# Kernel tuning notes

Measured on AMD Instinct MI355X. Metric: run time of the kernel, lower is better.

## Reference

```python
import jax, jax.numpy as jnp
import numpy as np


def setup_inputs() -> dict:
    key = jax.random.key(0)
    k1, k2 = jax.random.split(key)
    B, N, M, D = 4, 8192, 8192, 3
    preds = jax.random.normal(k1, (B, M, D), dtype=jnp.float32)
    gts = jax.random.normal(k2, (B, N, D), dtype=jnp.float32)
    return {"preds": preds, "gts": gts, "c": 1}


def reference(preds, gts, c):
    # x = gts [B, Nx, D], y = preds [B, Ny, D] (matches batch_pairwise_dist(gts, preds))
    x, y = gts, preds
    cf = jnp.asarray(c, dtype=x.dtype)
    # P[b, i, j] = ||x_i||^2 + ||y_j||^2 - 2 <x_i, y_j>  (squared Euclidean distance)
    zz = jnp.einsum('bnd,bmd->bnm', x, y)            # [B, Nx, Ny]
    rx = jnp.sum(x * x, axis=-1)[:, :, None]          # [B, Nx, 1]
    ry = jnp.sum(y * y, axis=-1)[:, None, :]          # [B, 1, Ny]
    P = rx + ry - 2.0 * zz                            # [B, Nx, Ny]

    def huber(v):
        return jnp.where(v < cf, 0.5 * v * v, cf * v - 0.5 * cf * cf)

    loss_1 = jnp.sum(huber(jnp.min(P, axis=1)))       # min over Nx (gts side)
    loss_2 = jnp.sum(huber(jnp.min(P, axis=2)))       # min over Ny (preds side)
    return loss_1 + loss_2
```

## Files before the change

kernel.cpp:

```cpp
#include <hip/hip_runtime.h>
#include <math.h>

typedef _Float16 f16x8 __attribute__((ext_vector_type(8)));
typedef float f32x16 __attribute__((ext_vector_type(16)));

#define TILE 1024

__device__ __forceinline__ float decode_scalar(const int* p) {
    int i = *p;
    if (i > -16777216 && i < 16777216) return (float)i;
    return __int_as_float(i);
}
__device__ __forceinline__ float min3f(float a, float b, float c) {
    float d;
    asm("v_min3_f32 %0, %1, %2, %3" : "=v"(d) : "v"(a), "v"(b), "v"(c));
    return d;
}

__device__ __forceinline__ f16x8 make_afrag(float x, float y, float z, int half) {
    const float rn = fmaf(x, x, fmaf(y, y, z * z));
    const float ax = -2.f * x, ay = -2.f * y, az = -2.f * z;
    const _Float16 ahx = (_Float16)ax, ahy = (_Float16)ay, ahz = (_Float16)az;
    const _Float16 alx = (_Float16)(ax - (float)ahx);
    const _Float16 aly = (_Float16)(ay - (float)ahy);
    const _Float16 alz = (_Float16)(az - (float)ahz);
    const _Float16 rh = (_Float16)rn, rl = (_Float16)(rn - (float)rh);
    const _Float16 one = (_Float16)1.f;
    if (half == 0) return (f16x8){ahx, ahy, ahz, alx, aly, alz, ahx, ahy};
    return (f16x8){ahz, alx, aly, alz, rh, rl, one, one};
}
__device__ __forceinline__ void make_bfrags(float x, float y, float z,
                                            f16x8* b0, f16x8* b1) {
    const float rn = fmaf(x, x, fmaf(y, y, z * z));
    const _Float16 bhx = (_Float16)x, bhy = (_Float16)y, bhz = (_Float16)z;
    const _Float16 blx = (_Float16)(x - (float)bhx);
    const _Float16 bly = (_Float16)(y - (float)bhy);
    const _Float16 blz = (_Float16)(z - (float)bhz);
    const _Float16 rh = (_Float16)rn, rl = (_Float16)(rn - (float)rh);
    const _Float16 one = (_Float16)1.f;
    *b0 = (f16x8){bhx, bhy, bhz, bhx, bhy, bhz, blx, bly};
    *b1 = (f16x8){blz, blx, bly, blz, one, one, rh, rl};
}

__global__ __launch_bounds__(256) void nn_mfma(
    const float* __restrict__ preds, const float* __restrict__ gts,
    int M, int N, int B, int rsplit, int Qstride, float* __restrict__ part)
{
    const int zc    = blockIdx.z;
    const int dir   = zc / rsplit;
    const int chunk = zc - dir * rsplit;
    const int b     = blockIdx.y;

    const int Q = dir ? N : M;
    const int R = dir ? M : N;
    const float* __restrict__ qraw = (dir ? gts : preds) + (size_t)b * Q * 3;
    const float* __restrict__ rraw = (dir ? preds : gts) + (size_t)b * R * 3;

    const int q0blk = blockIdx.x * 256;
    if (q0blk >= Q) return;
    const int tid  = threadIdx.x;
    const int lane = tid & 63, w = tid >> 6;
    const int q0   = q0blk + w * 64;
    const int lrow = lane & 31, lh = lane >> 5;

    float ax = 0.f, ay = 0.f, az = 0.f, bx = 0.f, by = 0.f, bz = 0.f;
    const int qa = q0 + lrow, qb = q0 + 32 + lrow;
    if (qa < Q) { const float* s = qraw + (size_t)qa * 3; ax = s[0]; ay = s[1]; az = s[2]; }
    if (qb < Q) { const float* s = qraw + (size_t)qb * 3; bx = s[0]; by = s[1]; bz = s[2]; }
    const f16x8 af0 = make_afrag(ax, ay, az, lh);
    const f16x8 af1 = make_afrag(bx, by, bz, lh);

    __shared__ f16x8 sB[TILE * 2];

    f32x16 rm0, rm1;
    #pragma unroll
    for (int j = 0; j < 16; ++j) { rm0[j] = INFINITY; rm1[j] = INFINITY; }

    const int tilesTotal = (R + TILE - 1) / TILE;
    const int tpc = (tilesTotal + rsplit - 1) / rsplit;
    const int t0 = chunk * tpc;
    const int t1 = min(tilesTotal, t0 + tpc);

    for (int tt = t0; tt < t1; ++tt) {
        const int s0 = tt * TILE;
        __syncthreads();
        #pragma unroll
        for (int k = 0; k < 4; ++k) {
            const int p  = tid + k * 256;
            const int gi = s0 + p;
            f16x8 b0, b1;
            if (gi < R) {
                const float* s = rraw + (size_t)gi * 3;
                make_bfrags(s[0], s[1], s[2], &b0, &b1);
            } else {
                const _Float16 z0 = (_Float16)0.f, one = (_Float16)1.f;
                const _Float16 big = (_Float16)60000.f;
                b0 = (f16x8){z0, z0, z0, z0, z0, z0, z0, z0};
                b1 = (f16x8){z0, z0, z0, z0, one, one, big, z0};
            }
            const int g = p >> 5, sl = p & 31;
            sB[g * 64 + sl]      = b0;
            sB[g * 64 + 32 + sl] = b1;
        }
        __syncthreads();

        #pragma unroll 1
        for (int tp = 0; tp < TILE / 64; ++tp) {
            const f16x8 cb0 = sB[2 * tp * 64 + lane];
            const f16x8 cb1 = sB[(2 * tp + 1) * 64 + lane];
            f32x16 dA, dB;
            asm volatile(
                "v_mfma_f32_32x32x16_f16 %0, %2, %3, 0\n\t"
                "v_mfma_f32_32x32x16_f16 %1, %2, %4, 0\n\t"
                "s_nop 7\n\t"
                "s_nop 7\n\t"
                "s_nop 7\n\t"
                "s_nop 7"
                : "=&v"(dA), "=&v"(dB)
                : "v"(af0), "v"(cb0), "v"(cb1));
            #pragma unroll
            for (int j = 0; j < 16; ++j) rm0[j] = min3f(dA[j], dB[j], rm0[j]);
            f32x16 dC, dD;
            asm volatile(
                "v_mfma_f32_32x32x16_f16 %0, %2, %3, 0\n\t"
                "v_mfma_f32_32x32x16_f16 %1, %2, %4, 0\n\t"
                "s_nop 7\n\t"
                "s_nop 7\n\t"
                "s_nop 7\n\t"
                "s_nop 7"
                : "=&v"(dC), "=&v"(dD)
                : "v"(af1), "v"(cb0), "v"(cb1));
            #pragma unroll
            for (int j = 0; j < 16; ++j) rm1[j] = min3f(dC[j], dD[j], rm1[j]);
        }
    }

    __syncthreads();
    float* sT = (float*)&sB[0] + (w << 11);
    const int c  = lrow;
    const int sw = 4 * (c & 7);

    #pragma unroll
    for (int jj = 0; jj < 4; ++jj) {
        const int qb0 = jj * 8 + 4 * lh;
        float4 v0 = { rm0[4*jj], rm0[4*jj+1], rm0[4*jj+2], rm0[4*jj+3] };
        *(float4*)&sT[c * 64 + (qb0 ^ sw)] = v0;
        const int qb1 = 32 + qb0;
        float4 v1 = { rm1[4*jj], rm1[4*jj+1], rm1[4*jj+2], rm1[4*jj+3] };
        *(float4*)&sT[c * 64 + (qb1 ^ sw)] = v1;
    }
    __syncthreads();

    float t16[16];
    #pragma unroll
    for (int cc = 0; cc < 16; ++cc) {
        const float va = sT[(2*cc)     * 64 + (lane ^ (4 * ((2*cc)     & 7)))];
        const float vb = sT[(2*cc + 1) * 64 + (lane ^ (4 * ((2*cc + 1) & 7)))];
        t16[cc] = fminf(va, vb);
    }
    #pragma unroll
    for (int s = 8; s > 0; s >>= 1)
        #pragma unroll
        for (int i = 0; i < 8; ++i)
            if (i < s) t16[i] = fminf(t16[i], t16[i + s]);

    const size_t pbase = (((size_t)dir * B + b) * rsplit + chunk) * (size_t)Qstride + q0;
    part[pbase + lane] = t16[0];
}

__global__ __launch_bounds__(1024) void huber_reduce(
    const float* __restrict__ part, const int* __restrict__ cptr,
    int M, int N, int B, int rsplit, int Qstride, float* __restrict__ out)
{
    const int dir = blockIdx.z;
    const int b   = blockIdx.y;
    const int Q   = dir ? N : M;
    const int tid = threadIdx.x;
    const int j   = blockIdx.x * 1024 + tid;

    float h = 0.f;
    if (j < Q) {
        const size_t base = (((size_t)dir * B + b) * rsplit) * (size_t)Qstride + j;
        float v = part[base];
        #pragma unroll 4
        for (int k = 1; k < rsplit; ++k) v = fminf(v, part[base + (size_t)k * Qstride]);
        const float c = decode_scalar(cptr);
        h = (v < c) ? (0.5f * v * v) : fmaf(c, v, -0.5f * c * c);
    }

    #pragma unroll
    for (int off = 32; off > 0; off >>= 1) h += __shfl_down(h, off, 64);

    __shared__ float wsum[16];
    if ((tid & 63) == 0) wsum[tid >> 6] = h;
    __syncthreads();
    if (tid < 64) {
        float t = (tid < 16) ? wsum[tid] : 0.f;
        #pragma unroll
        for (int off = 8; off > 0; off >>= 1) t += __shfl_down(t, off, 64);
        if (tid == 0) atomicAdd(out, t);
    }
}

extern "C" void kernel_launch(void* const* d_in, const int* in_sizes, int n_in,
                              void* d_out, int out_size, void* d_ws, size_t ws_size,
                              hipStream_t stream) {
    const float* preds = (const float*)d_in[0];
    const float* gts   = (const float*)d_in[1];
    const int*   cptr  = (const int*)d_in[2];

    const int B = 4, D = 3;
    const int M = in_sizes[0] / (B * D);
    const int N = in_sizes[1] / (B * D);
    const int Qmax = (M > N) ? M : N;
    const int Qstride = (Qmax + 255) & ~255;
    const int rsplit = 4;

    float* part = (float*)d_ws;
    hipMemsetAsync(d_out, 0, (size_t)out_size * sizeof(float), stream);

    dim3 g1(Qstride / 256, B, 2 * rsplit);
    nn_mfma<<<g1, 256, 0, stream>>>(preds, gts, M, N, B, rsplit, Qstride, part);

    dim3 g2((Qmax + 1023) / 1024, B, 2);
    huber_reduce<<<g2, 1024, 0, stream>>>(part, cptr, M, N, B, rsplit, Qstride,
                                          (float*)d_out);
}
```

Baseline: 33.21 us.

## Software-pipeline MFMA tile loop so min3 reductions overlap next MFMAs

Restructures the inner tile loop so the MFMA outputs of one step are min-reduced while the next step's MFMAs are in flight. It adds a prologue and epilogue and drops the hard-coded s_nop padding after each MFMA pair. Scheduling barriers fix the ordering of shared-memory loads, min3 reductions and MFMA issue. The aim is to remove idle cycles spent waiting on MFMA results. The risk is that hazard wait-states are no longer guaranteed for inline-asm MFMA results read soon after issue, especially in the epilogue, and the extra live accumulators raise register pressure.

```diff
diff --git a/kernel.cpp b/kernel.cpp
--- a/kernel.cpp
+++ b/kernel.cpp
@@ -16,6 +16,7 @@
     asm("v_min3_f32 %0, %1, %2, %3" : "=v"(d) : "v"(a), "v"(b), "v"(c));
     return d;
 }
+#define SBAR() __builtin_amdgcn_sched_barrier(0)
 
 __device__ __forceinline__ f16x8 make_afrag(float x, float y, float z, int half) {
     const float rn = fmaf(x, x, fmaf(y, y, z * z));
@@ -104,35 +105,45 @@
         }
         __syncthreads();
 
+        const f16x8* pl = sB + lane;
+        f16x8 cb0 = pl[0];
+        f16x8 cb1 = pl[64];
+        f32x16 dA, dB, dC, dD;
+        asm volatile(
+            "v_mfma_f32_32x32x16_f16 %0, %2, %3, 0\n\t"
+            "v_mfma_f32_32x32x16_f16 %1, %2, %4, 0"
+            : "=&v"(dA), "=&v"(dB) : "v"(af0), "v"(cb0), "v"(cb1));
+        asm volatile(
+            "v_mfma_f32_32x32x16_f16 %0, %2, %3, 0\n\t"
+            "v_mfma_f32_32x32x16_f16 %1, %2, %4, 0"
+            : "=&v"(dC), "=&v"(dD) : "v"(af1), "v"(cb0), "v"(cb1));
+
         #pragma unroll 1
-        for (int tp = 0; tp < TILE / 64; ++tp) {
-            const f16x8 cb0 = sB[2 * tp * 64 + lane];
-            const f16x8 cb1 = sB[(2 * tp + 1) * 64 + lane];
-            f32x16 dA, dB;
+        for (int tp = 1; tp < TILE / 64; ++tp) {
+            SBAR();
+            cb0 = pl[tp * 128];
+            cb1 = pl[tp * 128 + 64];
+            #pragma unroll
+            for (int j = 0; j < 16; ++j) rm0[j] = min3f(dA[j], dB[j], rm0[j]);
+            SBAR();
             asm volatile(
                 "v_mfma_f32_32x32x16_f16 %0, %2, %3, 0\n\t"
-                "v_mfma_f32_32x32x16_f16 %1, %2, %4, 0\n\t"
-                "s_nop 7\n\t"
-                "s_nop 7\n\t"
-                "s_nop 7\n\t"
-                "s_nop 7"
-                : "=&v"(dA), "=&v"(dB)
-                : "v"(af0), "v"(cb0), "v"(cb1));
+                "v_mfma_f32_32x32x16_f16 %1, %2, %4, 0"
+                : "=&v"(dA), "=&v"(dB) : "v"(af0), "v"(cb0), "v"(cb1));
+            SBAR();
             #pragma unroll
-            for (int j = 0; j < 16; ++j) rm0[j] = min3f(dA[j], dB[j], rm0[j]);
-            f32x16 dC, dD;
+            for (int j = 0; j < 16; ++j) rm1[j] = min3f(dC[j], dD[j], rm1[j]);
+            SBAR();
             asm volatile(
                 "v_mfma_f32_32x32x16_f16 %0, %2, %3, 0\n\t"
-                "v_mfma_f32_32x32x16_f16 %1, %2, %4, 0\n\t"
-                "s_nop 7\n\t"
-                "s_nop 7\n\t"
-                "s_nop 7\n\t"
-                "s_nop 7"
-                : "=&v"(dC), "=&v"(dD)
-                : "v"(af1), "v"(cb0), "v"(cb1));
-            #pragma unroll
-            for (int j = 0; j < 16; ++j) rm1[j] = min3f(dC[j], dD[j], rm1[j]);
+                "v_mfma_f32_32x32x16_f16 %1, %2, %4, 0"
+                : "=&v"(dC), "=&v"(dD) : "v"(af1), "v"(cb0), "v"(cb1));
         }
+        SBAR();
+        #pragma unroll
+        for (int j = 0; j < 16; ++j) rm0[j] = min3f(dA[j], dB[j], rm0[j]);
+        #pragma unroll
+        for (int j = 0; j < 16; ++j) rm1[j] = min3f(dC[j], dD[j], rm1[j]);
     }
 
     __syncthreads();
```

After: 31.56 us (median of 2 runs). -5.0%, faster.

## Load reference points directly per wave with register prefetch instead of LDS tiles

Applied to the files above, without the earlier changes.

The shared-memory tiling of reference-point fragments is replaced. Each wave now reads two reference points per iteration straight from global memory, prefetches the next pair into registers, and packs the f16 hi/lo fragments in-lane. This removes the block-wide barriers and LDS traffic around each tile, and a barrier in the final per-wave transpose is dropped. The cost is that all four waves now repeat the packing arithmetic and issue redundant strided global loads that depend on cache hits. The split of the reference set across chunks is now done at 64-point granularity.

```diff
diff --git a/kernel.cpp b/kernel.cpp
--- a/kernel.cpp
+++ b/kernel.cpp
@@ -3,8 +3,6 @@
 
 typedef _Float16 f16x8 __attribute__((ext_vector_type(8)));
 typedef float f32x16 __attribute__((ext_vector_type(16)));
-
-#define TILE 1024
 
 __device__ __forceinline__ float decode_scalar(const int* p) {
     int i = *p;
@@ -29,17 +27,19 @@
     if (half == 0) return (f16x8){ahx, ahy, ahz, alx, aly, alz, ahx, ahy};
     return (f16x8){ahz, alx, aly, alz, rh, rl, one, one};
 }
-__device__ __forceinline__ void make_bfrags(float x, float y, float z,
-                                            f16x8* b0, f16x8* b1) {
-    const float rn = fmaf(x, x, fmaf(y, y, z * z));
+
+__device__ __forceinline__ f16x8 pack_lane(float x, float y, float z,
+                                           int oob, int lh) {
+    float rn = fmaf(x, x, fmaf(y, y, z * z));
+    rn = oob ? 60000.f : rn;
     const _Float16 bhx = (_Float16)x, bhy = (_Float16)y, bhz = (_Float16)z;
     const _Float16 blx = (_Float16)(x - (float)bhx);
     const _Float16 bly = (_Float16)(y - (float)bhy);
     const _Float16 blz = (_Float16)(z - (float)bhz);
     const _Float16 rh = (_Float16)rn, rl = (_Float16)(rn - (float)rh);
     const _Float16 one = (_Float16)1.f;
-    *b0 = (f16x8){bhx, bhy, bhz, bhx, bhy, bhz, blx, bly};
-    *b1 = (f16x8){blz, blx, bly, blz, one, one, rh, rl};
+    if (lh == 0) return (f16x8){bhx, bhy, bhz, bhx, bhy, bhz, blx, bly};
+    return (f16x8){blz, blx, bly, blz, one, one, rh, rl};
 }
 
 __global__ __launch_bounds__(256) void nn_mfma(
@@ -56,11 +56,9 @@
     const float* __restrict__ qraw = (dir ? gts : preds) + (size_t)b * Q * 3;
     const float* __restrict__ rraw = (dir ? preds : gts) + (size_t)b * R * 3;
 
-    const int q0blk = blockIdx.x * 256;
-    if (q0blk >= Q) return;
     const int tid  = threadIdx.x;
     const int lane = tid & 63, w = tid >> 6;
-    const int q0   = q0blk + w * 64;
+    const int q0   = blockIdx.x * 256 + w * 64;
     const int lrow = lane & 31, lh = lane >> 5;
 
     float ax = 0.f, ay = 0.f, az = 0.f, bx = 0.f, by = 0.f, bz = 0.f;
@@ -70,44 +68,39 @@
     const f16x8 af0 = make_afrag(ax, ay, az, lh);
     const f16x8 af1 = make_afrag(bx, by, bz, lh);
 
-    __shared__ f16x8 sB[TILE * 2];
+    __shared__ float sTall[4 * 2048];
 
     f32x16 rm0, rm1;
     #pragma unroll
     for (int j = 0; j < 16; ++j) { rm0[j] = INFINITY; rm1[j] = INFINITY; }
 
-    const int tilesTotal = (R + TILE - 1) / TILE;
-    const int tpc = (tilesTotal + rsplit - 1) / rsplit;
-    const int t0 = chunk * tpc;
-    const int t1 = min(tilesTotal, t0 + tpc);
-
-    for (int tt = t0; tt < t1; ++tt) {
-        const int s0 = tt * TILE;
-        __syncthreads();
-        #pragma unroll
-        for (int k = 0; k < 4; ++k) {
-            const int p  = tid + k * 256;
-            const int gi = s0 + p;
-            f16x8 b0, b1;
-            if (gi < R) {
-                const float* s = rraw + (size_t)gi * 3;
-                make_bfrags(s[0], s[1], s[2], &b0, &b1);
-            } else {
-                const _Float16 z0 = (_Float16)0.f, one = (_Float16)1.f;
-                const _Float16 big = (_Float16)60000.f;
-                b0 = (f16x8){z0, z0, z0, z0, z0, z0, z0, z0};
-                b1 = (f16x8){z0, z0, z0, z0, one, one, big, z0};
+    const int gran = (((R + 63) >> 6) + rsplit - 1) / rsplit;
+    const int g0 = chunk * gran;
+    const int iters = min(gran, ((R + 63) >> 6) - g0);
+
+    if (iters > 0) {
+        int pt = g0 * 64 + lrow;
+        int o0 = (pt >= R), o1 = (pt + 32 >= R);
+        const float* s0 = rraw + (size_t)min(pt, R - 1) * 3;
+        const float* s1 = rraw + (size_t)min(pt + 32, R - 1) * 3;
+        float cx0 = s0[0], cy0 = s0[1], cz0 = s0[2];
+        float cx1 = s1[0], cy1 = s1[1], cz1 = s1[2];
+
+        #pragma unroll 1
+        for (int tp = 0; tp < iters; ++tp) {
+            const float x0 = cx0, y0 = cy0, z0 = cz0;
+            const float x1 = cx1, y1 = cy1, z1 = cz1;
+            const int f0 = o0, f1 = o1;
+            if (tp + 1 < iters) {
+                pt += 64;
+                o0 = (pt >= R); o1 = (pt + 32 >= R);
+                const float* n0 = rraw + (size_t)min(pt, R - 1) * 3;
+                const float* n1 = rraw + (size_t)min(pt + 32, R - 1) * 3;
+                cx0 = n0[0]; cy0 = n0[1]; cz0 = n0[2];
+                cx1 = n1[0]; cy1 = n1[1]; cz1 = n1[2];
             }
-            const int g = p >> 5, sl = p & 31;
-            sB[g * 64 + sl]      = b0;
-            sB[g * 64 + 32 + sl] = b1;
-        }
-        __syncthreads();
-
-        #pragma unroll 1
-        for (int tp = 0; tp < TILE / 64; ++tp) {
-            const f16x8 cb0 = sB[2 * tp * 64 + lane];
-            const f16x8 cb1 = sB[(2 * tp + 1) * 64 + lane];
+            const f16x8 cb0 = pack_lane(x0, y0, z0, f0, lh);
+            const f16x8 cb1 = pack_lane(x1, y1, z1, f1, lh);
             f32x16 dA, dB;
             asm volatile(
                 "v_mfma_f32_32x32x16_f16 %0, %2, %3, 0\n\t"
@@ -135,8 +128,7 @@
         }
     }
 
-    __syncthreads();
-    float* sT = (float*)&sB[0] + (w << 11);
+    float* sT = sTall + (w << 11);
     const int c  = lrow;
     const int sw = 4 * (c & 7);
 
@@ -149,7 +141,6 @@
         float4 v1 = { rm1[4*jj], rm1[4*jj+1], rm1[4*jj+2], rm1[4*jj+3] };
         *(float4*)&sT[c * 64 + (qb1 ^ sw)] = v1;
     }
-    __syncthreads();
 
     float t16[16];
     #pragma unroll
```

Result: slower. 43.75 us (+31.7%).

## Halve query rows per wave to double block count in MFMA NN kernel

Applied to the files above, without the earlier changes.

Each wave now processes 32 query points with a single A fragment instead of 64 with two, and the grid doubles along x to cover the same queries. This halves the per-wave accumulator registers and MFMA work per reference tile, giving twice as many blocks to spread across CUs. In exchange, each staged reference tile in shared memory is reused by half as many queries, so tile building and LDS reads per MFMA roughly double.

```diff
diff --git a/kernel.cpp b/kernel.cpp
--- a/kernel.cpp
+++ b/kernel.cpp
@@ -56,25 +56,23 @@
     const float* __restrict__ qraw = (dir ? gts : preds) + (size_t)b * Q * 3;
     const float* __restrict__ rraw = (dir ? preds : gts) + (size_t)b * R * 3;
 
-    const int q0blk = blockIdx.x * 256;
+    const int q0blk = blockIdx.x * 128;
     if (q0blk >= Q) return;
     const int tid  = threadIdx.x;
     const int lane = tid & 63, w = tid >> 6;
-    const int q0   = q0blk + w * 64;
+    const int q0   = q0blk + w * 32;
     const int lrow = lane & 31, lh = lane >> 5;
 
-    float ax = 0.f, ay = 0.f, az = 0.f, bx = 0.f, by = 0.f, bz = 0.f;
-    const int qa = q0 + lrow, qb = q0 + 32 + lrow;
+    float ax = 0.f, ay = 0.f, az = 0.f;
+    const int qa = q0 + lrow;
     if (qa < Q) { const float* s = qraw + (size_t)qa * 3; ax = s[0]; ay = s[1]; az = s[2]; }
-    if (qb < Q) { const float* s = qraw + (size_t)qb * 3; bx = s[0]; by = s[1]; bz = s[2]; }
-    const f16x8 af0 = make_afrag(ax, ay, az, lh);
-    const f16x8 af1 = make_afrag(bx, by, bz, lh);
+    const f16x8 af = make_afrag(ax, ay, az, lh);
 
     __shared__ f16x8 sB[TILE * 2];
 
-    f32x16 rm0, rm1;
-    #pragma unroll
-    for (int j = 0; j < 16; ++j) { rm0[j] = INFINITY; rm1[j] = INFINITY; }
+    f32x16 rm;
+    #pragma unroll
+    for (int j = 0; j < 16; ++j) rm[j] = INFINITY;
 
     const int tilesTotal = (R + TILE - 1) / TILE;
     const int tpc = (tilesTotal + rsplit - 1) / rsplit;
@@ -104,10 +102,11 @@
         }
         __syncthreads();
 
+        const f16x8* pl = sB + lane;
         #pragma unroll 1
         for (int tp = 0; tp < TILE / 64; ++tp) {
-            const f16x8 cb0 = sB[2 * tp * 64 + lane];
-            const f16x8 cb1 = sB[(2 * tp + 1) * 64 + lane];
+            const f16x8 cb0 = pl[tp * 128];
+            const f16x8 cb1 = pl[tp * 128 + 64];
             f32x16 dA, dB;
             asm volatile(
                 "v_mfma_f32_32x32x16_f16 %0, %2, %3, 0\n\t"
@@ -117,45 +116,30 @@
                 "s_nop 7\n\t"
                 "s_nop 7"
                 : "=&v"(dA), "=&v"(dB)
-                : "v"(af0), "v"(cb0), "v"(cb1));
+                : "v"(af), "v"(cb0), "v"(cb1));
             #pragma unroll
-            for (int j = 0; j < 16; ++j) rm0[j] = min3f(dA[j], dB[j], rm0[j]);
-            f32x16 dC, dD;
-            asm volatile(
-                "v_mfma_f32_32x32x16_f16 %0, %2, %3, 0\n\t"
-                "v_mfma_f32_32x32x16_f16 %1, %2, %4, 0\n\t"
-                "s_nop 7\n\t"
-                "s_nop 7\n\t"
-                "s_nop 7\n\t"
-                "s_nop 7"
-                : "=&v"(dC), "=&v"(dD)
-                : "v"(af1), "v"(cb0), "v"(cb1));
-            #pragma unroll
-            for (int j = 0; j < 16; ++j) rm1[j] = min3f(dC[j], dD[j], rm1[j]);
+            for (int j = 0; j < 16; ++j) rm[j] = min3f(dA[j], dB[j], rm[j]);
         }
     }
 
     __syncthreads();
-    float* sT = (float*)&sB[0] + (w << 11);
+    float* sT = (float*)&sB[0] + (w << 10);
     const int c  = lrow;
     const int sw = 4 * (c & 7);
 
     #pragma unroll
     for (int jj = 0; jj < 4; ++jj) {
-        const int qb0 = jj * 8 + 4 * lh;
-        float4 v0 = { rm0[4*jj], rm0[4*jj+1], rm0[4*jj+2], rm0[4*jj+3] };
-        *(float4*)&sT[c * 64 + (qb0 ^ sw)] = v0;
-        const int qb1 = 32 + qb0;
-        float4 v1 = { rm1[4*jj], rm1[4*jj+1], rm1[4*jj+2], rm1[4*jj+3] };
-        *(float4*)&sT[c * 64 + (qb1 ^ sw)] = v1;
+        const int rb = jj * 8 + 4 * lh;
+        float4 v = { rm[4*jj], rm[4*jj+1], rm[4*jj+2], rm[4*jj+3] };
+        *(float4*)&sT[c * 32 + (rb ^ sw)] = v;
     }
     __syncthreads();
 
     float t16[16];
     #pragma unroll
     for (int cc = 0; cc < 16; ++cc) {
-        const float va = sT[(2*cc)     * 64 + (lane ^ (4 * ((2*cc)     & 7)))];
-        const float vb = sT[(2*cc + 1) * 64 + (lane ^ (4 * ((2*cc + 1) & 7)))];
+        const float va = sT[(2*cc)     * 32 + (lrow ^ (4 * ((2*cc)     & 7)))];
+        const float vb = sT[(2*cc + 1) * 32 + (lrow ^ (4 * ((2*cc + 1) & 7)))];
         t16[cc] = fminf(va, vb);
     }
     #pragma unroll
@@ -164,8 +148,10 @@
         for (int i = 0; i < 8; ++i)
             if (i < s) t16[i] = fminf(t16[i], t16[i + s]);
 
-    const size_t pbase = (((size_t)dir * B + b) * rsplit + chunk) * (size_t)Qstride + q0;
-    part[pbase + lane] = t16[0];
+    if (lh == 0) {
+        const size_t pbase = (((size_t)dir * B + b) * rsplit + chunk) * (size_t)Qstride + q0;
+        part[pbase + lrow] = t16[0];
+    }
 }
 
 __global__ __launch_bounds__(1024) void huber_reduce(
@@ -219,7 +205,7 @@
     float* part = (float*)d_ws;
     hipMemsetAsync(d_out, 0, (size_t)out_size * sizeof(float), stream);
 
-    dim3 g1(Qstride / 256, B, 2 * rsplit);
+    dim3 g1(Qstride / 128, B, 2 * rsplit);
     nn_mfma<<<g1, 256, 0, stream>>>(preds, gts, M, N, B, rsplit, Qstride, part);
 
     dim3 g2((Qmax + 1023) / 1024, B, 2);
```

After: 36.29 us. +9.3%, slower.
